# Kernel optimization log

Hardware: AMD Instinct MI355X
Metric: run time of the kernel (lower is better)

Reference implementation:

```python
import jax, jax.numpy as jnp
import numpy as np

SEQ = 2048
D_MODEL = 2048
N_HEADS = 16
D_HEAD = D_MODEL // N_HEADS
GN_EPS = 1e-5


def apply_xpos(x, inv=False, base=10000.0, scale_base=512.0):
    # x: (sqlen, d_head). Standard xPos: rotary embedding with exponential length scale.
    s, d = x.shape
    half = d // 2
    freqs = 1.0 / (base ** (jnp.arange(half, dtype=jnp.float32) / half))
    pos = jnp.arange(s, dtype=jnp.float32)
    ang = pos[:, None] * freqs[None, :]                       # (s, half)
    sin, cos = jnp.sin(ang), jnp.cos(ang)
    scale = ((jnp.arange(half, dtype=jnp.float32) + 0.4 * d) / (1.4 * d)) ** (pos[:, None] / scale_base)
    if inv:
        scale = 1.0 / scale
    x1, x2 = x[:, :half], x[:, half:]
    y1 = (x1 * cos - x2 * sin) * scale
    y2 = (x1 * sin + x2 * cos) * scale
    return jnp.concatenate([y1, y2], axis=-1)


def setup_inputs() -> dict:
    key = jax.random.key(0)
    ks = jax.random.split(key, 8)
    s = D_MODEL ** -0.5
    return {
        "x": jax.random.normal(ks[0], (SEQ, D_MODEL), jnp.float32),
        "state": jax.random.normal(ks[1], (N_HEADS, D_HEAD, D_HEAD), jnp.float32) * 0.1,
        "Wqkv": jax.random.normal(ks[2], (3 * D_MODEL, D_MODEL), jnp.float32) * s,
        "Walpha": jax.random.normal(ks[3], (1, D_MODEL), jnp.float32) * s,
        "gn_w": jnp.ones((D_MODEL,), jnp.float32),
        "gn_b": jnp.zeros((D_MODEL,), jnp.float32),
        "Wgate": jax.random.normal(ks[4], (D_MODEL, D_MODEL), jnp.float32) * s,
        "Wout": jax.random.normal(ks[5], (D_MODEL, D_MODEL), jnp.float32) * s,
    }


def reference(x, state, Wqkv, Walpha, gn_w, gn_b, Wgate, Wout):
    sqlen = x.shape[0]
    # qkv projection -> (3, H, s, Dh)
    qkv = (x @ Wqkv.T).reshape(sqlen, 3, N_HEADS, D_HEAD).transpose(1, 2, 0, 3)
    q, k, v = qkv[0], qkv[1], qkv[2]
    q = jax.vmap(apply_xpos)(q)
    k = jax.vmap(lambda t: apply_xpos(t, inv=True))(k)

    alphas = -jnp.log1p(jnp.exp(-(x @ Walpha.T)))             # log-sigmoid, (s, 1)
    k = (1.0 - jnp.exp(alphas)) * k                            # broadcast (s,1) over (H,s,Dh)
    a = jnp.cumsum(alphas, axis=0)                             # (s, 1)

    # Decay matrix; mask BEFORE exp (equivalent to tril-after since upper is zeroed,
    # but avoids overflow in exp for the upper triangle).
    tril = jnp.tril(jnp.ones((sqlen, sqlen), bool))
    Delta = jnp.exp(jnp.where(tril, a - a.T, -jnp.inf))        # (s, s)

    attn = jnp.tril(jnp.einsum('hid,hjd,ij->hij', q, k, Delta))  # (H, s, s)
    ret = jnp.einsum('hij,hjd->ihd', attn, v)                    # (s, H, Dh)

    new_state = jnp.exp(a[-1]) * state                           # (H, Dh, Dh)
    ret = ret + jnp.einsum('hid,hde->ihe', q, new_state)
    new_state = new_state + jnp.einsum('hid,hie,i->hde', k, v, jnp.exp(a[::-1, 0]))

    # GroupNorm(n_heads groups) over d_model, per token
    r = ret.reshape(sqlen, N_HEADS, D_HEAD)
    mu = r.mean(-1, keepdims=True)
    var = r.var(-1, keepdims=True)
    r = (r - mu) * jax.lax.rsqrt(var + GN_EPS)
    ret = r.reshape(sqlen, D_MODEL) * gn_w + gn_b

    gate = jax.nn.swish(ret @ Wgate.T)
    out = (gate * ret) @ Wout.T
    return out, new_state
```

## Files before the change

kernel.cpp:

```cpp
#include <hip/hip_runtime.h>

#define SEQ 2048
#define DM 2048
#define NH 16
#define DH 128

typedef float f32x4 __attribute__((ext_vector_type(4)));
typedef short s16x8 __attribute__((ext_vector_type(8)));

__device__ __forceinline__ ushort f2bf(float f) {
    unsigned u = __builtin_bit_cast(unsigned, f);
    return (ushort)((u + 0x7FFFu + ((u >> 16) & 1u)) >> 16);
}
__device__ __forceinline__ float bf2f(ushort u) {
    return __builtin_bit_cast(float, (unsigned)u << 16);
}
__device__ __forceinline__ void gload_lds16(const void* g, void* l) {
    __builtin_amdgcn_global_load_lds((const __attribute__((address_space(1))) void*)g,
                                     (__attribute__((address_space(3))) void*)l, 16, 0, 0);
}

__global__ __launch_bounds__(256) void k_xprep(const float* __restrict__ x,
                                               const float* __restrict__ wal,
                                               ushort* __restrict__ x_bf,
                                               float* __restrict__ z) {
    int row = blockIdx.x, t = threadIdx.x;
    const float4* xr = (const float4*)(x + (size_t)row * DM);
    const float4* wa = (const float4*)wal;
    float4 v0 = xr[t], v1 = xr[t + 256];
    float4 w0 = wa[t], w1 = wa[t + 256];
    float s = v0.x * w0.x + v0.y * w0.y + v0.z * w0.z + v0.w * w0.w
            + v1.x * w1.x + v1.y * w1.y + v1.z * w1.z + v1.w * w1.w;
    ushort4 o0, o1;
    o0.x = f2bf(v0.x); o0.y = f2bf(v0.y); o0.z = f2bf(v0.z); o0.w = f2bf(v0.w);
    o1.x = f2bf(v1.x); o1.y = f2bf(v1.y); o1.z = f2bf(v1.z); o1.w = f2bf(v1.w);
    ushort4* xb = (ushort4*)(x_bf + (size_t)row * DM);
    xb[t] = o0; xb[t + 256] = o1;
    __shared__ float red[4];
    int lane = t & 63, wv = t >> 6;
    #pragma unroll
    for (int off = 32; off; off >>= 1) s += __shfl_down(s, off);
    if (lane == 0) red[wv] = s;
    __syncthreads();
    if (t == 0) z[row] = red[0] + red[1] + red[2] + red[3];
}

__global__ __launch_bounds__(256) void k_prep2(const float* __restrict__ z,
                                               float* __restrict__ a,
                                               float* __restrict__ wrev,
                                               float* __restrict__ kscale,
                                               float* __restrict__ exp_alast,
                                               const float* __restrict__ Wqkv,
                                               ushort* __restrict__ Wqkv_bf,
                                               float* __restrict__ tsin,
                                               float* __restrict__ tcos,
                                               float* __restrict__ tsc) {
    int b = blockIdx.x, t = threadIdx.x;
    if (b == 0) {
        __shared__ float sh[SEQ];
        __shared__ float csum[256];
        for (int i = t; i < SEQ; i += 256) {
            float al = -log1pf(expf(-z[i]));
            sh[i] = al;
            kscale[i] = 1.f - expf(al);
        }
        __syncthreads();
        int base = t * 8;
        float run = 0.f, loc[8];
        #pragma unroll
        for (int j = 0; j < 8; j++) { run += sh[base + j]; loc[j] = run; }
        csum[t] = run;
        __syncthreads();
        if (t == 0) {
            float r = 0.f;
            for (int i = 0; i < 256; i++) { float v = csum[i]; csum[i] = r; r += v; }
        }
        __syncthreads();
        float off = csum[t];
        #pragma unroll
        for (int j = 0; j < 8; j++) { float av = loc[j] + off; sh[base + j] = av; a[base + j] = av; }
        __syncthreads();
        for (int i = t; i < SEQ; i += 256) wrev[i] = expf(sh[SEQ - 1 - i]);
        if (t == 0) *exp_alast = expf(sh[SEQ - 1]);
    } else if (b < 1 + 3 * DM * DM / 4 / 256) {
        int i = (b - 1) * 256 + t;
        float4 v = ((const float4*)Wqkv)[i];
        ushort4 o;
        o.x = f2bf(v.x); o.y = f2bf(v.y); o.z = f2bf(v.z); o.w = f2bf(v.w);
        ((ushort4*)Wqkv_bf)[i] = o;
    } else {
        int idx = (b - 1 - 3 * DM * DM / 4 / 256) * 256 + t;
        int i = idx >> 6, j = idx & 63;
        float freq = powf(10000.f, -(float)j / 64.f);
        float ang = (float)i * freq;
        tsin[idx] = sinf(ang);
        tcos[idx] = cosf(ang);
        tsc[idx]  = powf(((float)j + 51.2f) / 179.2f, (float)i / 512.f);
    }
}

template <int EPI, int STORE_BF16>
__global__ __launch_bounds__(256) void k_gemm_mfma(
    const ushort* __restrict__ A,
    const ushort* __restrict__ B,
    void* __restrict__ Cv, int ldc,
    const ushort* __restrict__ aux,
    int K)
{
    (void)K;
    __shared__ __align__(16) ushort As[128 * 64];
    __shared__ __align__(16) ushort Bs[128 * 64];
    int bx = blockIdx.x, by = blockIdx.y;
    {
        int id = by * 16 + bx;
        int xcd = id & 7, local = id >> 3;
        int lbx = local & 7, lby = local >> 3;
        bx = (xcd & 1) * 8 + lbx;
        by = (xcd >> 1) * 4 + lby;
    }
    int bm = by * 128, bn = bx * 128;
    int tid = threadIdx.x;
    int w = tid >> 6, l = tid & 63;
    int wr = w >> 1, wc = w & 1;
    int lr = l & 15, kg = l >> 4;

    int srow = w * 32 + (l >> 3);
    int scol = ((l & 7) ^ (l >> 3)) * 8;
    const ushort* ga = A + (size_t)(bm + srow) * DM + scol;
    const ushort* gb = B + (size_t)(bn + srow) * DM + scol;
    ushort* la = As + (w * 32) * 64;
    ushort* lb = Bs + (w * 32) * 64;

    f32x4 acc[4][4] = {};

    for (int k0 = 0; k0 < DM; k0 += 64) {
        __syncthreads();
        #pragma unroll
        for (int g = 0; g < 4; g++) {
            gload_lds16(ga + (size_t)(g * 8) * DM + k0, la + g * 8 * 64);
            gload_lds16(gb + (size_t)(g * 8) * DM + k0, lb + g * 8 * 64);
        }
        __syncthreads();

        #pragma unroll
        for (int kk = 0; kk < 2; kk++) {
            s16x8 af[4], bfr[4];
            #pragma unroll
            for (int m = 0; m < 4; m++) {
                int row = wr * 64 + m * 16 + lr;
                af[m] = *(const s16x8*)(As + row * 64 + (((kk * 4 + kg) ^ (lr & 7)) * 8));
            }
            #pragma unroll
            for (int n = 0; n < 4; n++) {
                int row = wc * 64 + n * 16 + lr;
                bfr[n] = *(const s16x8*)(Bs + row * 64 + (((kk * 4 + kg) ^ (lr & 7)) * 8));
            }
            #pragma unroll
            for (int m = 0; m < 4; m++)
                #pragma unroll
                for (int n = 0; n < 4; n++)
                    asm volatile("v_mfma_f32_16x16x32_bf16 %0, %1, %2, %0"
                                 : "+v"(acc[m][n]) : "v"(af[m]), "v"(bfr[n]));
        }
    }
    asm volatile("s_nop 7\n\ts_nop 7\n\ts_nop 7" ::: );

    #pragma unroll
    for (int m = 0; m < 4; m++) {
        int grow = bm + wr * 64 + m * 16 + kg * 4;
        #pragma unroll
        for (int n = 0; n < 4; n++) {
            int gcol = bn + wc * 64 + n * 16 + lr;
            #pragma unroll
            for (int j = 0; j < 4; j++) {
                float c = acc[m][n][j];
                size_t off = (size_t)(grow + j) * ldc + gcol;
                if (EPI == 1) {
                    float sig = 1.f / (1.f + __expf(-c));
                    c = c * sig * bf2f(aux[off]);
                }
                if (STORE_BF16) ((ushort*)Cv)[off] = f2bf(c);
                else            ((float*)Cv)[off] = c;
            }
        }
    }
}

__global__ __launch_bounds__(256) void k_gemm_qkv(
    const ushort* __restrict__ A,
    const ushort* __restrict__ B,
    const float* __restrict__ tsin,
    const float* __restrict__ tcos,
    const float* __restrict__ tsc,
    const float* __restrict__ kscale,
    const float* __restrict__ wrev,
    ushort* __restrict__ qh,
    ushort* __restrict__ kh,
    ushort* __restrict__ vth,
    ushort* __restrict__ kwtr)
{
    __shared__ __align__(16) char smem[33024];
    ushort* As = (ushort*)smem;
    ushort* Bs = (ushort*)(smem + 16384);
    int bx = blockIdx.x, by = blockIdx.y;
    {
        int id = by * 48 + bx;
        int xcd = id & 7, local = id >> 3;
        int lbx = local % 12, lby = local / 12;
        bx = (xcd & 3) * 12 + lbx;
        by = (xcd >> 2) * 8 + lby;
    }
    int bm = by * 128, bn = bx * 128;
    int tid = threadIdx.x;
    int w = tid >> 6, l = tid & 63;
    int wr = w >> 1, wc = w & 1;
    int lr = l & 15, kg = l >> 4;

    int srow = w * 32 + (l >> 3);
    int scol = ((l & 7) ^ (l >> 3)) * 8;
    const ushort* ga = A + (size_t)(bm + srow) * DM + scol;
    const ushort* gb = B + (size_t)(bn + srow) * DM + scol;
    ushort* la = As + (w * 32) * 64;
    ushort* lb = Bs + (w * 32) * 64;

    f32x4 acc[4][4] = {};

    for (int k0 = 0; k0 < DM; k0 += 64) {
        __syncthreads();
        #pragma unroll
        for (int g = 0; g < 4; g++) {
            gload_lds16(ga + (size_t)(g * 8) * DM + k0, la + g * 8 * 64);
            gload_lds16(gb + (size_t)(g * 8) * DM + k0, lb + g * 8 * 64);
        }
        __syncthreads();

        #pragma unroll
        for (int kk = 0; kk < 2; kk++) {
            s16x8 af[4], bfr[4];
            #pragma unroll
            for (int m = 0; m < 4; m++) {
                int row = wr * 64 + m * 16 + lr;
                af[m] = *(const s16x8*)(As + row * 64 + (((kk * 4 + kg) ^ (lr & 7)) * 8));
            }
            #pragma unroll
            for (int n = 0; n < 4; n++) {
                int row = wc * 64 + n * 16 + lr;
                bfr[n] = *(const s16x8*)(Bs + row * 64 + (((kk * 4 + kg) ^ (lr & 7)) * 8));
            }
            #pragma unroll
            for (int m = 0; m < 4; m++)
                #pragma unroll
                for (int n = 0; n < 4; n++)
                    asm volatile("v_mfma_f32_16x16x32_bf16 %0, %1, %2, %0"
                                 : "+v"(acc[m][n]) : "v"(af[m]), "v"(bfr[n]));
        }
    }
    asm volatile("s_nop 7\n\ts_nop 7\n\ts_nop 7" ::: );

    __syncthreads();
    ushort* S = (ushort*)smem;
    #pragma unroll
    for (int m = 0; m < 4; m++) {
        int row = wr * 64 + m * 16 + kg * 4;
        #pragma unroll
        for (int n = 0; n < 4; n++) {
            int col = wc * 64 + n * 16 + lr;
            #pragma unroll
            for (int j = 0; j < 4; j++)
                S[(row + j) * 129 + col] = f2bf(acc[m][n][j]);
        }
    }
    __syncthreads();

    int type = bn >> 11;
    int h = (bn & 2047) >> 7;

    if (type < 2) {
        #pragma unroll 4
        for (int rr = 0; rr < 32; rr++) {
            int r = w * 32 + rr;
            int i = bm + r;
            float sn = tsin[i * 64 + l], cs = tcos[i * 64 + l], sc = tsc[i * 64 + l];
            float v1 = bf2f(S[r * 129 + l]), v2 = bf2f(S[r * 129 + l + 64]);
            float r1 = v1 * cs - v2 * sn, r2 = v1 * sn + v2 * cs;
            size_t ob = ((size_t)h * SEQ + i) * DH;
            if (type == 0) {
                qh[ob + l]      = f2bf(r1 * sc);
                qh[ob + l + 64] = f2bf(r2 * sc);
            } else {
                float ks = kscale[i], wv = wrev[i];
                float isc = 1.f / sc;
                float k1 = r1 * isc * ks, k2 = r2 * isc * ks;
                kh[ob + l]      = f2bf(k1);
                kh[ob + l + 64] = f2bf(k2);
                S[r * 129 + l]      = f2bf(k1 * wv);
                S[r * 129 + l + 64] = f2bf(k2 * wv);
            }
        }
    }
    if (type >= 1) {
        __syncthreads();
        ushort* dstT = (type == 1) ? kwtr : vth;
        #pragma unroll 4
        for (int dd = 0; dd < 32; dd++) {
            int d = w * 32 + dd;
            ushort2 o;
            o.x = S[(2 * l) * 129 + d];
            o.y = S[(2 * l + 1) * 129 + d];
            *(ushort2*)(dstT + ((size_t)h * DH + d) * SEQ + bm + 2 * l) = o;
        }
    }
}

#define NUNITS 48
__constant__ unsigned char U_QT[NUNITS] = {
    31,31,30,15, 30,29,29,28,14, 28,27,27,26,13, 26,25,25,24,12,
    24,23,23,22,11, 22,21,21,20,10, 20,19,19,18,9, 18,17,17,16,8,
    16,7,6,5,4,3,2,1,0};
__constant__ unsigned char U_T0[NUNITS] = {
    0,16,0,0, 16,0,15,0,0, 15,0,14,0,0, 14,0,13,0,0,
    13,0,12,0,0, 12,0,11,0,0, 11,0,10,0,0, 10,0,9,0,0,
    9,0,0,0,0,0,0,0,0};
__constant__ unsigned char U_T1[NUNITS] = {
    16,32,16,16, 31,15,30,15,15, 29,14,28,14,14, 27,13,26,13,13,
    25,12,24,12,12, 23,11,22,11,11, 21,10,20,10,10, 19,9,18,9,9,
    17,8,7,6,5,4,3,2,1};

__global__ __launch_bounds__(256) void k_attn_mega(
    const ushort* __restrict__ qh,
    const ushort* __restrict__ kh,
    const ushort* __restrict__ vth,
    const ushort* __restrict__ kwtr,
    const float* __restrict__ a,
    float* __restrict__ ret,
    float* __restrict__ ret2,
    float* __restrict__ part,
    const float* __restrict__ gw,
    const float* __restrict__ gb,
    ushort* __restrict__ retn_bf,
    const float* __restrict__ Wgate,
    ushort* __restrict__ Wgate_bf,
    const float* __restrict__ Wout,
    ushort* __restrict__ Wout_bf)
{
    __shared__ __align__(16) char smem[81920];
    int h, u;
    {
        int id = blockIdx.y * NH + blockIdx.x;
        int xcd = id & 7, local = id >> 3;
        h = xcd * 2 + (local >> 6);
        u = local & 63;
    }
    int tid = threadIdx.x;
    int w = tid >> 6, l = tid & 63;
    int lr = l & 15, kg = l >> 4;

    if (u >= 56) {
        int id = (u - 56) * NH + h;
        const float4* g0 = (const float4*)Wgate;
        const float4* g1 = (const float4*)Wout;
        #pragma unroll 4
        for (int it = 0; it < 32; it++) {
            int idx = id * 8192 + it * 256 + tid;
            float4 v = g0[idx];
            ushort4 o;
            o.x = f2bf(v.x); o.y = f2bf(v.y); o.z = f2bf(v.z); o.w = f2bf(v.w);
            ((ushort4*)Wgate_bf)[idx] = o;
            v = g1[idx];
            o.x = f2bf(v.x); o.y = f2bf(v.y); o.z = f2bf(v.z); o.w = f2bf(v.w);
            ((ushort4*)Wout_bf)[idx] = o;
        }
        return;
    }
    if (u >= 48) {
        int ch = u - 48;
        const ushort* A = kwtr + (size_t)h * DH * SEQ + ch * (SEQ / 8);
        const ushort* B = vth  + (size_t)h * DH * SEQ + ch * (SEQ / 8);
        ushort* As = (ushort*)smem;
        ushort* Bs = (ushort*)(smem + 8192);
        int wr = w >> 1, wc = w & 1;
        int srow = w * 16 + (l >> 2);
        int scol = (l & 3) * 8;
        const ushort* ga0 = A + (size_t)srow * SEQ + scol;
        const ushort* ga1 = A + (size_t)(64 + srow) * SEQ + scol;
        const ushort* gb0 = B + (size_t)srow * SEQ + scol;
        const ushort* gb1 = B + (size_t)(64 + srow) * SEQ + scol;
        ushort* la0 = As + w * 512;
        ushort* la1 = As + 2048 + w * 512;
        ushort* lb0 = Bs + w * 512;
        ushort* lb1 = Bs + 2048 + w * 512;
        f32x4 acc[4][4] = {};
        for (int k0 = 0; k0 < SEQ / 8; k0 += 32) {
            __syncthreads();
            gload_lds16(ga0 + k0, la0);
            gload_lds16(ga1 + k0, la1);
            gload_lds16(gb0 + k0, lb0);
            gload_lds16(gb1 + k0, lb1);
            __syncthreads();
            s16x8 af[4], bfr[4];
            #pragma unroll
            for (int m = 0; m < 4; m++)
                af[m] = *(const s16x8*)(As + (wr * 64 + m * 16 + lr) * 32 + kg * 8);
            #pragma unroll
            for (int n = 0; n < 4; n++)
                bfr[n] = *(const s16x8*)(Bs + (wc * 64 + n * 16 + lr) * 32 + kg * 8);
            #pragma unroll
            for (int m = 0; m < 4; m++)
                #pragma unroll
                for (int n = 0; n < 4; n++)
                    asm volatile("v_mfma_f32_16x16x32_bf16 %0, %1, %2, %0"
                                 : "+v"(acc[m][n]) : "v"(af[m]), "v"(bfr[n]));
        }
        asm volatile("s_nop 7\n\ts_nop 7\n\ts_nop 7" ::: );
        float* p = part + ((size_t)ch * NH + h) * DH * DH;
        #pragma unroll
        for (int m = 0; m < 4; m++) {
            int grow = wr * 64 + m * 16 + kg * 4;
            #pragma unroll
            for (int n = 0; n < 4; n++) {
                int gcol = wc * 64 + n * 16 + lr;
                #pragma unroll
                for (int j = 0; j < 4; j++)
                    p[(size_t)(grow + j) * DH + gcol] = acc[m][n][j];
            }
        }
        return;
    }

    int qt = U_QT[u], t0 = U_T0[u], t1 = U_T1[u];
    int i0 = qt * 64;
    const ushort* Q  = qh  + (size_t)h * SEQ * DH;
    const ushort* K  = kh  + (size_t)h * SEQ * DH;
    const ushort* Vt = vth + (size_t)h * DH * SEQ;
#define KS(B) ((ushort*)(smem + (B) * 16384))
#define VS(B) ((ushort*)(smem + 32768 + (B) * 16384))
    char* Ps = smem + 65536;
    float* a_lds = (float*)(smem + 73728);

    int span = t1 * 64;
    for (int i = tid; i < span; i += 256) a_lds[i] = a[i];

    s16x8 qf[4];
    #pragma unroll
    for (int c = 0; c < 4; c++)
        qf[c] = *(const s16x8*)(Q + (size_t)(i0 + w * 16 + lr) * DH + c * 32 + kg * 8);
    float aq[4];
    #pragma unroll
    for (int r = 0; r < 4; r++) aq[r] = a[i0 + w * 16 + kg * 4 + r];

    f32x4 oacc[8] = {};

#define STAGE(T, B) do { int j0_ = (T) * 64;                                      \
    _Pragma("unroll") for (int g = 0; g < 4; g++) {                               \
        int row = w * 16 + g * 4 + (l >> 4);                                      \
        int cb = ((l & 15) * 16) ^ ((row & 7) << 4);                              \
        gload_lds16(K + (size_t)(j0_ + row) * DH + cb / 2,                        \
                    (char*)KS(B) + (w * 16 + g * 4) * 256); }                     \
    _Pragma("unroll") for (int g = 0; g < 4; g++) {                               \
        int e = w * 32 + g * 8 + (l >> 3);                                        \
        int cb = ((l & 7) * 16) ^ ((e & 7) << 4);                                 \
        gload_lds16(Vt + (size_t)e * SEQ + j0_ + cb / 2,                          \
                    (char*)VS(B) + (w * 32 + g * 8) * 128); }                     \
} while (0)

    STAGE(t0, 0);
    __syncthreads();

    for (int t = t0; t < t1; t++) {
        int cur = (t - t0) & 1;
        if (t + 1 < t1) {
            STAGE(t + 1, cur ^ 1);
            asm volatile("s_waitcnt vmcnt(8)" ::: "memory");
        } else {
            asm volatile("s_waitcnt vmcnt(0)" ::: "memory");
        }
        __builtin_amdgcn_s_barrier();

        f32x4 sacc[4] = {};
        __builtin_amdgcn_s_setprio(1);
        #pragma unroll
        for (int n = 0; n < 4; n++) {
            int krow = n * 16 + lr;
            #pragma unroll
            for (int c = 0; c < 4; c++) {
                s16x8 kf = *(const s16x8*)((const char*)KS(cur) + krow * 256 +
                            ((c * 64 + kg * 16) ^ ((krow & 7) << 4)));
                asm volatile("v_mfma_f32_16x16x32_bf16 %0, %1, %2, %0"
                             : "+v"(sacc[n]) : "v"(qf[c]), "v"(kf));
            }
        }
        __builtin_amdgcn_s_setprio(0);
        asm volatile("s_nop 7\n\ts_nop 7" ::: );

        int j0 = t * 64;
        float aref = a_lds[j0];
        float ei[4], ej[4];
        #pragma unroll
        for (int r = 0; r < 4; r++) ei[r] = __expf(aq[r] - aref);
        #pragma unroll
        for (int n = 0; n < 4; n++) ej[n] = __expf(aref - a_lds[j0 + n * 16 + lr]);
        bool diag = (t == qt);
        #pragma unroll
        for (int n = 0; n < 4; n++) {
            #pragma unroll
            for (int r = 0; r < 4; r++) {
                float wv = ei[r] * ej[n];
                if (diag)
                    wv = (n * 16 + lr <= w * 16 + kg * 4 + r) ? wv : 0.f;
                float p = sacc[n][r] * wv;
                int prow = w * 16 + kg * 4 + r;
                *(ushort*)(Ps + prow * 128 +
                           (((n * 16 + lr) * 2) ^ ((prow & 7) << 4))) = f2bf(p);
            }
        }
        __builtin_amdgcn_s_setprio(1);
        #pragma unroll
        for (int c2 = 0; c2 < 2; c2++) {
            int prow = w * 16 + lr;
            s16x8 pf = *(const s16x8*)((const char*)Ps + prow * 128 +
                        ((c2 * 64 + kg * 16) ^ ((prow & 7) << 4)));
            #pragma unroll
            for (int n2 = 0; n2 < 8; n2++) {
                int erow = n2 * 16 + lr;
                s16x8 vf = *(const s16x8*)((const char*)VS(cur) + erow * 128 +
                            ((c2 * 64 + kg * 16) ^ ((erow & 7) << 4)));
                asm volatile("v_mfma_f32_16x16x32_bf16 %0, %1, %2, %0"
                             : "+v"(oacc[n2]) : "v"(pf), "v"(vf));
            }
        }
        __builtin_amdgcn_s_setprio(0);
        asm volatile("s_waitcnt lgkmcnt(0)" ::: "memory");
        __builtin_amdgcn_s_barrier();
    }
#undef STAGE
    asm volatile("s_nop 7\n\ts_nop 7\n\ts_nop 7" ::: );

    if (qt < 16) {
        float gwr[8], gbr[8];
        #pragma unroll
        for (int n2 = 0; n2 < 8; n2++) {
            gwr[n2] = gw[h * DH + n2 * 16 + lr];
            gbr[n2] = gb[h * DH + n2 * 16 + lr];
        }
        #pragma unroll
        for (int j = 0; j < 4; j++) {
            float s = 0.f, sq = 0.f;
            #pragma unroll
            for (int n2 = 0; n2 < 8; n2++) { float v = oacc[n2][j]; s += v; sq += v * v; }
            #pragma unroll
            for (int off = 8; off; off >>= 1) {
                s  += __shfl_xor(s, off);
                sq += __shfl_xor(sq, off);
            }
            float mu = s * (1.f / 128.f);
            float var = sq * (1.f / 128.f) - mu * mu;
            float inv = rsqrtf(var + 1e-5f);
            int gi = i0 + w * 16 + kg * 4 + j;
            #pragma unroll
            for (int n2 = 0; n2 < 8; n2++) {
                float val = (oacc[n2][j] - mu) * inv * gwr[n2] + gbr[n2];
                retn_bf[(size_t)gi * DM + h * DH + n2 * 16 + lr] = f2bf(val);
            }
        }
    } else {
        float* dst = (t0 == 0) ? ret + (size_t)i0 * DM
                               : ret2 + (size_t)(i0 - 1024) * DM;
        #pragma unroll
        for (int n2 = 0; n2 < 8; n2++) {
            #pragma unroll
            for (int j = 0; j < 4; j++) {
                int ri = w * 16 + kg * 4 + j;
                dst[(size_t)ri * DM + h * DH + n2 * 16 + lr] = oacc[n2][j];
            }
        }
    }
}

__global__ __launch_bounds__(64) void k_gnorm(const float* __restrict__ ret,
                                              const float* __restrict__ ret2,
                                              const float* __restrict__ gw,
                                              const float* __restrict__ gb,
                                              ushort* __restrict__ retn_bf,
                                              const float* __restrict__ part,
                                              const float* __restrict__ state,
                                              const float* __restrict__ exp_alast,
                                              float* __restrict__ out_state) {
    int bx = blockIdx.x, h = blockIdx.y;
    int t = threadIdx.x;
    if (bx >= 1024) {
        int bx2 = bx - 1024;
        int idx4 = bx2 * 64 + t;
        size_t off = (size_t)h * (DH * DH / 4) + idx4;
        float ea = *exp_alast;
        float4 s4 = ((const float4*)state)[off];
        float4 acc;
        acc.x = s4.x * ea; acc.y = s4.y * ea; acc.z = s4.z * ea; acc.w = s4.w * ea;
        #pragma unroll
        for (int ch = 0; ch < 8; ch++) {
            float4 p4 = ((const float4*)part)[((size_t)ch * NH) * (DH * DH / 4) + off];
            acc.x += p4.x; acc.y += p4.y; acc.z += p4.z; acc.w += p4.w;
        }
        ((float4*)out_state)[off] = acc;
        return;
    }
    int i = 1024 + bx;
    const float* r = ret + (size_t)i * DM + h * DH;
    const float* r2 = ret2 + (size_t)(i - 1024) * DM + h * DH;
    float v0 = r[t] + r2[t], v1 = r[t + 64] + r2[t + 64];
    float s = v0 + v1, sq = v0 * v0 + v1 * v1;
    #pragma unroll
    for (int off = 32; off; off >>= 1) { s += __shfl_xor(s, off); sq += __shfl_xor(sq, off); }
    float mu = s * (1.f / 128.f);
    float var = sq * (1.f / 128.f) - mu * mu;
    float inv = rsqrtf(var + 1e-5f);
    ushort* o = retn_bf + (size_t)i * DM + h * DH;
    o[t]      = f2bf((v0 - mu) * inv * gw[h * DH + t]      + gb[h * DH + t]);
    o[t + 64] = f2bf((v1 - mu) * inv * gw[h * DH + t + 64] + gb[h * DH + t + 64]);
}

extern "C" void kernel_launch(void* const* d_in, const int* in_sizes, int n_in,
                              void* d_out, int out_size, void* d_ws, size_t ws_size,
                              hipStream_t stream) {
    (void)in_sizes; (void)n_in; (void)out_size; (void)ws_size;
    const float* x      = (const float*)d_in[0];
    const float* state  = (const float*)d_in[1];
    const float* Wqkv   = (const float*)d_in[2];
    const float* Walpha = (const float*)d_in[3];
    const float* gn_w   = (const float*)d_in[4];
    const float* gn_b   = (const float*)d_in[5];
    const float* Wgate  = (const float*)d_in[6];
    const float* Wout   = (const float*)d_in[7];
    float* out       = (float*)d_out;
    float* out_state = out + (size_t)SEQ * DM;

    char* base = (char*)d_ws;
    ushort* x_bf     = (ushort*)base;
    ushort* retn_bf  = (ushort*)base;
    ushort* Wqkv_bf  = (ushort*)(base + 8388608);
    float*  ret      = (float*)(base + 8388608);
    float*  ret2     = (float*)(base + 25165824);
    ushort* qh       = (ushort*)(base + 33554432);
    ushort* kh       = (ushort*)(base + 41943040);
    ushort* vth      = (ushort*)(base + 50331648);
    ushort* kwtr     = (ushort*)(base + 58720256);
    float*  part     = (float*)(base + 67108864);
    ushort* gr_bf    = (ushort*)(base + 67108864);
    float*  tsin     = (float*)(base + 75497472);
    float*  tcos     = (float*)(base + 75497472 + 524288);
    float*  tsc      = (float*)(base + 75497472 + 1048576);
    ushort* Wgate_bf = (ushort*)(base + 75497472);
    ushort* Wout_bf  = (ushort*)(base + 83886080);
    float*  smalls   = (float*)(base + 92274688);
    float* z = smalls, *a = z + SEQ, *wrev = a + SEQ, *kscale = wrev + SEQ, *exp_alast = kscale + SEQ;

    k_xprep<<<dim3(SEQ), dim3(256), 0, stream>>>(x, Walpha, x_bf, z);
    k_prep2<<<dim3(1 + 3 * DM * DM / 4 / 256 + SEQ * 64 / 256), dim3(256), 0, stream>>>(
        z, a, wrev, kscale, exp_alast, Wqkv, Wqkv_bf, tsin, tcos, tsc);
    k_gemm_qkv<<<dim3(48, SEQ / 128), dim3(256), 0, stream>>>(
        x_bf, Wqkv_bf, tsin, tcos, tsc, kscale, wrev, qh, kh, vth, kwtr);
    k_attn_mega<<<dim3(NH, 64), dim3(256), 0, stream>>>(
        qh, kh, vth, kwtr, a, ret, ret2, part,
        gn_w, gn_b, retn_bf, Wgate, Wgate_bf, Wout, Wout_bf);
    k_gnorm<<<dim3(1024 + 64, NH), dim3(64), 0, stream>>>(
        ret, ret2, gn_w, gn_b, retn_bf, part, state, exp_alast, out_state);
    k_gemm_mfma<1, 1><<<dim3(DM / 128, SEQ / 128), dim3(256), 0, stream>>>(
        retn_bf, Wgate_bf, gr_bf, DM, retn_bf, DM);
    k_gemm_mfma<0, 0><<<dim3(DM / 128, SEQ / 128), dim3(256), 0, stream>>>(
        gr_bf, Wout_bf, out, DM, nullptr, DM);
}
```

Before: 222.4 us.

## Fuse prep kernels and group-norm into producers via last-block atomic counters

New measurement: 447.2 us. 101% more time.

```diff
diff --git a/kernel.cpp b/kernel.cpp
--- a/kernel.cpp
+++ b/kernel.cpp
@@ -20,76 +20,84 @@
                                      (__attribute__((address_space(3))) void*)l, 16, 0, 0);
 }
 
-__global__ __launch_bounds__(256) void k_xprep(const float* __restrict__ x,
-                                               const float* __restrict__ wal,
-                                               ushort* __restrict__ x_bf,
-                                               float* __restrict__ z) {
-    int row = blockIdx.x, t = threadIdx.x;
-    const float4* xr = (const float4*)(x + (size_t)row * DM);
-    const float4* wa = (const float4*)wal;
-    float4 v0 = xr[t], v1 = xr[t + 256];
-    float4 w0 = wa[t], w1 = wa[t + 256];
-    float s = v0.x * w0.x + v0.y * w0.y + v0.z * w0.z + v0.w * w0.w
-            + v1.x * w1.x + v1.y * w1.y + v1.z * w1.z + v1.w * w1.w;
-    ushort4 o0, o1;
-    o0.x = f2bf(v0.x); o0.y = f2bf(v0.y); o0.z = f2bf(v0.z); o0.w = f2bf(v0.w);
-    o1.x = f2bf(v1.x); o1.y = f2bf(v1.y); o1.z = f2bf(v1.z); o1.w = f2bf(v1.w);
-    ushort4* xb = (ushort4*)(x_bf + (size_t)row * DM);
-    xb[t] = o0; xb[t + 256] = o1;
+__global__ __launch_bounds__(256) void k_mega_prep(
+    const float* __restrict__ x,
+    const float* __restrict__ wal,
+    ushort* __restrict__ x_bf,
+    float* __restrict__ z,
+    const float* __restrict__ Wqkv,
+    ushort* __restrict__ Wqkv_bf,
+    float* __restrict__ tsin,
+    float* __restrict__ tcos,
+    float* __restrict__ tsc,
+    float* __restrict__ a,
+    float* __restrict__ wrev,
+    float* __restrict__ kscale,
+    float* __restrict__ exp_alast,
+    int* __restrict__ ctrs)
+{
+    __shared__ float sh[SEQ];
+    __shared__ float csum[256];
     __shared__ float red[4];
-    int lane = t & 63, wv = t >> 6;
-    #pragma unroll
-    for (int off = 32; off; off >>= 1) s += __shfl_down(s, off);
-    if (lane == 0) red[wv] = s;
-    __syncthreads();
-    if (t == 0) z[row] = red[0] + red[1] + red[2] + red[3];
-}
-
-__global__ __launch_bounds__(256) void k_prep2(const float* __restrict__ z,
-                                               float* __restrict__ a,
-                                               float* __restrict__ wrev,
-                                               float* __restrict__ kscale,
-                                               float* __restrict__ exp_alast,
-                                               const float* __restrict__ Wqkv,
-                                               ushort* __restrict__ Wqkv_bf,
-                                               float* __restrict__ tsin,
-                                               float* __restrict__ tcos,
-                                               float* __restrict__ tsc) {
+    __shared__ int amLast;
     int b = blockIdx.x, t = threadIdx.x;
-    if (b == 0) {
-        __shared__ float sh[SEQ];
-        __shared__ float csum[256];
-        for (int i = t; i < SEQ; i += 256) {
-            float al = -log1pf(expf(-z[i]));
-            sh[i] = al;
-            kscale[i] = 1.f - expf(al);
-        }
-        __syncthreads();
-        int base = t * 8;
-        float run = 0.f, loc[8];
-        #pragma unroll
-        for (int j = 0; j < 8; j++) { run += sh[base + j]; loc[j] = run; }
-        csum[t] = run;
+    if (b < SEQ) {
+        const float4* xr = (const float4*)(x + (size_t)b * DM);
+        const float4* wa = (const float4*)wal;
+        float4 v0 = xr[t], v1 = xr[t + 256];
+        float4 w0 = wa[t], w1 = wa[t + 256];
+        float s = v0.x * w0.x + v0.y * w0.y + v0.z * w0.z + v0.w * w0.w
+                + v1.x * w1.x + v1.y * w1.y + v1.z * w1.z + v1.w * w1.w;
+        ushort4 o0, o1;
+        o0.x = f2bf(v0.x); o0.y = f2bf(v0.y); o0.z = f2bf(v0.z); o0.w = f2bf(v0.w);
+        o1.x = f2bf(v1.x); o1.y = f2bf(v1.y); o1.z = f2bf(v1.z); o1.w = f2bf(v1.w);
+        ushort4* xb = (ushort4*)(x_bf + (size_t)b * DM);
+        xb[t] = o0; xb[t + 256] = o1;
+        int lane = t & 63, wv = t >> 6;
+        #pragma unroll
+        for (int off = 32; off; off >>= 1) s += __shfl_down(s, off);
+        if (lane == 0) red[wv] = s;
         __syncthreads();
         if (t == 0) {
-            float r = 0.f;
-            for (int i = 0; i < 256; i++) { float v = csum[i]; csum[i] = r; r += v; }
-        }
-        __syncthreads();
-        float off = csum[t];
-        #pragma unroll
-        for (int j = 0; j < 8; j++) { float av = loc[j] + off; sh[base + j] = av; a[base + j] = av; }
-        __syncthreads();
-        for (int i = t; i < SEQ; i += 256) wrev[i] = expf(sh[SEQ - 1 - i]);
-        if (t == 0) *exp_alast = expf(sh[SEQ - 1]);
-    } else if (b < 1 + 3 * DM * DM / 4 / 256) {
-        int i = (b - 1) * 256 + t;
+            z[b] = red[0] + red[1] + red[2] + red[3];
+            __threadfence();
+            amLast = (atomicAdd(&ctrs[0], 1) == SEQ - 1);
+        }
+        __syncthreads();
+        if (amLast) {
+            __threadfence();
+            for (int i = t; i < SEQ; i += 256) {
+                float al = -log1pf(expf(-z[i]));
+                sh[i] = al;
+                kscale[i] = 1.f - expf(al);
+            }
+            __syncthreads();
+            int base = t * 8;
+            float run = 0.f, loc[8];
+            #pragma unroll
+            for (int j = 0; j < 8; j++) { run += sh[base + j]; loc[j] = run; }
+            csum[t] = run;
+            __syncthreads();
+            if (t == 0) {
+                float r = 0.f;
+                for (int i = 0; i < 256; i++) { float v = csum[i]; csum[i] = r; r += v; }
+            }
+            __syncthreads();
+            float off = csum[t];
+            #pragma unroll
+            for (int j = 0; j < 8; j++) { float av = loc[j] + off; sh[base + j] = av; a[base + j] = av; }
+            __syncthreads();
+            for (int i = t; i < SEQ; i += 256) wrev[i] = expf(sh[SEQ - 1 - i]);
+            if (t == 0) *exp_alast = expf(sh[SEQ - 1]);
+        }
+    } else if (b < SEQ + 3 * DM * DM / 4 / 256) {
+        int i = (b - SEQ) * 256 + t;
         float4 v = ((const float4*)Wqkv)[i];
         ushort4 o;
         o.x = f2bf(v.x); o.y = f2bf(v.y); o.z = f2bf(v.z); o.w = f2bf(v.w);
         ((ushort4*)Wqkv_bf)[i] = o;
     } else {
-        int idx = (b - 1 - 3 * DM * DM / 4 / 256) * 256 + t;
+        int idx = (b - SEQ - 3 * DM * DM / 4 / 256) * 256 + t;
         int i = idx >> 6, j = idx & 63;
         float freq = powf(10000.f, -(float)j / 64.f);
         float ang = (float)i * freq;
@@ -341,9 +349,14 @@
     const float* __restrict__ Wgate,
     ushort* __restrict__ Wgate_bf,
     const float* __restrict__ Wout,
-    ushort* __restrict__ Wout_bf)
+    ushort* __restrict__ Wout_bf,
+    const float* __restrict__ state,
+    const float* __restrict__ exp_alast,
+    float* __restrict__ out_state,
+    int* __restrict__ ctrs)
 {
     __shared__ __align__(16) char smem[81920];
+    __shared__ int amLast;
     int h, u;
     {
         int id = blockIdx.y * NH + blockIdx.x;
@@ -424,6 +437,28 @@
                     p[(size_t)(grow + j) * DH + gcol] = acc[m][n][j];
             }
         }
+        __threadfence();
+        if (tid == 0) amLast = (atomicAdd(&ctrs[272 + h], 1) == 7);
+        __syncthreads();
+        if (amLast) {
+            __threadfence();
+            float ea = *exp_alast;
+            #pragma unroll 4
+            for (int it = 0; it < 16; it++) {
+                int idx4 = it * 256 + tid;
+                size_t off2 = (size_t)h * 4096 + idx4;
+                float4 s4 = ((const float4*)state)[off2];
+                float4 acc2;
+                acc2.x = s4.x * ea; acc2.y = s4.y * ea;
+                acc2.z = s4.z * ea; acc2.w = s4.w * ea;
+                #pragma unroll
+                for (int c2 = 0; c2 < 8; c2++) {
+                    float4 p4 = ((const float4*)part)[(size_t)c2 * NH * 4096 + off2];
+                    acc2.x += p4.x; acc2.y += p4.y; acc2.z += p4.z; acc2.w += p4.w;
+                }
+                ((float4*)out_state)[off2] = acc2;
+            }
+        }
         return;
     }
 
@@ -573,49 +608,34 @@
                 dst[(size_t)ri * DM + h * DH + n2 * 16 + lr] = oacc[n2][j];
             }
         }
-    }
-}
-
-__global__ __launch_bounds__(64) void k_gnorm(const float* __restrict__ ret,
-                                              const float* __restrict__ ret2,
-                                              const float* __restrict__ gw,
-                                              const float* __restrict__ gb,
-                                              ushort* __restrict__ retn_bf,
-                                              const float* __restrict__ part,
-                                              const float* __restrict__ state,
-                                              const float* __restrict__ exp_alast,
-                                              float* __restrict__ out_state) {
-    int bx = blockIdx.x, h = blockIdx.y;
-    int t = threadIdx.x;
-    if (bx >= 1024) {
-        int bx2 = bx - 1024;
-        int idx4 = bx2 * 64 + t;
-        size_t off = (size_t)h * (DH * DH / 4) + idx4;
-        float ea = *exp_alast;
-        float4 s4 = ((const float4*)state)[off];
-        float4 acc;
-        acc.x = s4.x * ea; acc.y = s4.y * ea; acc.z = s4.z * ea; acc.w = s4.w * ea;
-        #pragma unroll
-        for (int ch = 0; ch < 8; ch++) {
-            float4 p4 = ((const float4*)part)[((size_t)ch * NH) * (DH * DH / 4) + off];
-            acc.x += p4.x; acc.y += p4.y; acc.z += p4.z; acc.w += p4.w;
-        }
-        ((float4*)out_state)[off] = acc;
-        return;
-    }
-    int i = 1024 + bx;
-    const float* r = ret + (size_t)i * DM + h * DH;
-    const float* r2 = ret2 + (size_t)(i - 1024) * DM + h * DH;
-    float v0 = r[t] + r2[t], v1 = r[t + 64] + r2[t + 64];
-    float s = v0 + v1, sq = v0 * v0 + v1 * v1;
-    #pragma unroll
-    for (int off = 32; off; off >>= 1) { s += __shfl_xor(s, off); sq += __shfl_xor(sq, off); }
-    float mu = s * (1.f / 128.f);
-    float var = sq * (1.f / 128.f) - mu * mu;
-    float inv = rsqrtf(var + 1e-5f);
-    ushort* o = retn_bf + (size_t)i * DM + h * DH;
-    o[t]      = f2bf((v0 - mu) * inv * gw[h * DH + t]      + gb[h * DH + t]);
-    o[t + 64] = f2bf((v1 - mu) * inv * gw[h * DH + t + 64] + gb[h * DH + t + 64]);
+        __threadfence();
+        if (tid == 0) amLast = (atomicAdd(&ctrs[16 + h * 16 + (qt - 16)], 1) == 1);
+        __syncthreads();
+        if (amLast) {
+            __threadfence();
+            float gw0 = gw[h * DH + l], gw1 = gw[h * DH + l + 64];
+            float gb0 = gb[h * DH + l], gb1 = gb[h * DH + l + 64];
+            for (int rr = 0; rr < 16; rr++) {
+                int i = i0 + w * 16 + rr;
+                const float* r  = ret  + (size_t)i * DM + h * DH;
+                const float* r2 = ret2 + (size_t)(i - 1024) * DM + h * DH;
+                float v0 = r[l] + r2[l];
+                float v1 = r[l + 64] + r2[l + 64];
+                float s = v0 + v1, sq = v0 * v0 + v1 * v1;
+                #pragma unroll
+                for (int off = 32; off; off >>= 1) {
+                    s  += __shfl_xor(s, off);
+                    sq += __shfl_xor(sq, off);
+                }
+                float mu = s * (1.f / 128.f);
+                float var = sq * (1.f / 128.f) - mu * mu;
+                float inv = rsqrtf(var + 1e-5f);
+                ushort* o = retn_bf + (size_t)i * DM + h * DH;
+                o[l]      = f2bf((v0 - mu) * inv * gw0 + gb0);
+                o[l + 64] = f2bf((v1 - mu) * inv * gw1 + gb1);
+            }
+        }
+    }
 }
 
 extern "C" void kernel_launch(void* const* d_in, const int* in_sizes, int n_in,
@@ -652,17 +672,18 @@
     ushort* Wout_bf  = (ushort*)(base + 83886080);
     float*  smalls   = (float*)(base + 92274688);
     float* z = smalls, *a = z + SEQ, *wrev = a + SEQ, *kscale = wrev + SEQ, *exp_alast = kscale + SEQ;
-
-    k_xprep<<<dim3(SEQ), dim3(256), 0, stream>>>(x, Walpha, x_bf, z);
-    k_prep2<<<dim3(1 + 3 * DM * DM / 4 / 256 + SEQ * 64 / 256), dim3(256), 0, stream>>>(
-        z, a, wrev, kscale, exp_alast, Wqkv, Wqkv_bf, tsin, tcos, tsc);
+    int*   ctrs      = (int*)(base + 92274688 + 36864);
+
+    hipMemsetAsync(ctrs, 0, 4096, stream);
+    k_mega_prep<<<dim3(SEQ + 3 * DM * DM / 4 / 256 + SEQ * 64 / 256), dim3(256), 0, stream>>>(
+        x, Walpha, x_bf, z, Wqkv, Wqkv_bf, tsin, tcos, tsc,
+        a, wrev, kscale, exp_alast, ctrs);
     k_gemm_qkv<<<dim3(48, SEQ / 128), dim3(256), 0, stream>>>(
         x_bf, Wqkv_bf, tsin, tcos, tsc, kscale, wrev, qh, kh, vth, kwtr);
     k_attn_mega<<<dim3(NH, 64), dim3(256), 0, stream>>>(
         qh, kh, vth, kwtr, a, ret, ret2, part,
-        gn_w, gn_b, retn_bf, Wgate, Wgate_bf, Wout, Wout_bf);
-    k_gnorm<<<dim3(1024 + 64, NH), dim3(64), 0, stream>>>(
-        ret, ret2, gn_w, gn_b, retn_bf, part, state, exp_alast, out_state);
+        gn_w, gn_b, retn_bf, Wgate, Wgate_bf, Wout, Wout_bf,
+        state, exp_alast, out_state, ctrs);
     k_gemm_mfma<1, 1><<<dim3(DM / 128, SEQ / 128), dim3(256), 0, stream>>>(
         retn_bf, Wgate_bf, gr_bf, DM, retn_bf, DM);
     k_gemm_mfma<0, 0><<<dim3(DM / 128, SEQ / 128), dim3(256), 0, stream>>>(
```

## Move Wout bf16 conversion into QKV GEMM launch and widen gnorm blocks

Applied to the files above, without the earlier changes.

Result: no change. 223.1 us (+0.4%).

```diff
diff --git a/kernel.cpp b/kernel.cpp
--- a/kernel.cpp
+++ b/kernel.cpp
@@ -197,21 +197,36 @@
     ushort* __restrict__ qh,
     ushort* __restrict__ kh,
     ushort* __restrict__ vth,
-    ushort* __restrict__ kwtr)
+    ushort* __restrict__ kwtr,
+    const float* __restrict__ Wout,
+    ushort* __restrict__ Wout_bf)
 {
+    int tid = threadIdx.x;
+    if (blockIdx.x >= 768) {
+        int cid = blockIdx.x - 768;
+        const float4* g1 = (const float4*)Wout;
+        #pragma unroll 4
+        for (int it = 0; it < 64; it++) {
+            int idx = cid * 16384 + it * 256 + tid;
+            float4 v = g1[idx];
+            ushort4 o;
+            o.x = f2bf(v.x); o.y = f2bf(v.y); o.z = f2bf(v.z); o.w = f2bf(v.w);
+            ((ushort4*)Wout_bf)[idx] = o;
+        }
+        return;
+    }
     __shared__ __align__(16) char smem[33024];
     ushort* As = (ushort*)smem;
     ushort* Bs = (ushort*)(smem + 16384);
-    int bx = blockIdx.x, by = blockIdx.y;
+    int bx, by;
     {
-        int id = by * 48 + bx;
+        int id = blockIdx.x;
         int xcd = id & 7, local = id >> 3;
         int lbx = local % 12, lby = local / 12;
         bx = (xcd & 3) * 12 + lbx;
         by = (xcd >> 2) * 8 + lby;
     }
     int bm = by * 128, bn = bx * 128;
-    int tid = threadIdx.x;
     int w = tid >> 6, l = tid & 63;
     int wr = w >> 1, wc = w & 1;
     int lr = l & 15, kg = l >> 4;
@@ -339,36 +354,30 @@
     const float* __restrict__ gb,
     ushort* __restrict__ retn_bf,
     const float* __restrict__ Wgate,
-    ushort* __restrict__ Wgate_bf,
-    const float* __restrict__ Wout,
-    ushort* __restrict__ Wout_bf)
+    ushort* __restrict__ Wgate_bf)
 {
     __shared__ __align__(16) char smem[81920];
     int h, u;
     {
         int id = blockIdx.y * NH + blockIdx.x;
         int xcd = id & 7, local = id >> 3;
-        h = xcd * 2 + (local >> 6);
-        u = local & 63;
+        h = xcd * 2 + (local / 60);
+        u = local % 60;
     }
     int tid = threadIdx.x;
     int w = tid >> 6, l = tid & 63;
     int lr = l & 15, kg = l >> 4;
 
     if (u >= 56) {
-        int id = (u - 56) * NH + h;
+        int s = (u - 56) * NH + h;
         const float4* g0 = (const float4*)Wgate;
-        const float4* g1 = (const float4*)Wout;
         #pragma unroll 4
-        for (int it = 0; it < 32; it++) {
-            int idx = id * 8192 + it * 256 + tid;
+        for (int it = 0; it < 64; it++) {
+            int idx = s * 16384 + it * 256 + tid;
             float4 v = g0[idx];
             ushort4 o;
             o.x = f2bf(v.x); o.y = f2bf(v.y); o.z = f2bf(v.z); o.w = f2bf(v.w);
             ((ushort4*)Wgate_bf)[idx] = o;
-            v = g1[idx];
-            o.x = f2bf(v.x); o.y = f2bf(v.y); o.z = f2bf(v.z); o.w = f2bf(v.w);
-            ((ushort4*)Wout_bf)[idx] = o;
         }
         return;
     }
@@ -576,37 +585,41 @@
     }
 }
 
-__global__ __launch_bounds__(64) void k_gnorm(const float* __restrict__ ret,
-                                              const float* __restrict__ ret2,
-                                              const float* __restrict__ gw,
-                                              const float* __restrict__ gb,
-                                              ushort* __restrict__ retn_bf,
-                                              const float* __restrict__ part,
-                                              const float* __restrict__ state,
-                                              const float* __restrict__ exp_alast,
-                                              float* __restrict__ out_state) {
+__global__ __launch_bounds__(256) void k_gnorm(const float* __restrict__ ret,
+                                               const float* __restrict__ ret2,
+                                               const float* __restrict__ gw,
+                                               const float* __restrict__ gb,
+                                               ushort* __restrict__ retn_bf,
+                                               const float* __restrict__ part,
+                                               const float* __restrict__ state,
+                                               const float* __restrict__ exp_alast,
+                                               float* __restrict__ out_state) {
     int bx = blockIdx.x, h = blockIdx.y;
     int t = threadIdx.x;
-    if (bx >= 1024) {
-        int bx2 = bx - 1024;
-        int idx4 = bx2 * 64 + t;
-        size_t off = (size_t)h * (DH * DH / 4) + idx4;
+    if (bx >= 256) {
+        int bx2 = bx - 256;
         float ea = *exp_alast;
-        float4 s4 = ((const float4*)state)[off];
-        float4 acc;
-        acc.x = s4.x * ea; acc.y = s4.y * ea; acc.z = s4.z * ea; acc.w = s4.w * ea;
-        #pragma unroll
-        for (int ch = 0; ch < 8; ch++) {
-            float4 p4 = ((const float4*)part)[((size_t)ch * NH) * (DH * DH / 4) + off];
-            acc.x += p4.x; acc.y += p4.y; acc.z += p4.z; acc.w += p4.w;
-        }
-        ((float4*)out_state)[off] = acc;
+        #pragma unroll
+        for (int it = 0; it < 4; it++) {
+            int idx4 = bx2 * 1024 + it * 256 + t;
+            size_t off = (size_t)h * (DH * DH / 4) + idx4;
+            float4 s4 = ((const float4*)state)[off];
+            float4 acc;
+            acc.x = s4.x * ea; acc.y = s4.y * ea; acc.z = s4.z * ea; acc.w = s4.w * ea;
+            #pragma unroll
+            for (int ch = 0; ch < 8; ch++) {
+                float4 p4 = ((const float4*)part)[((size_t)ch * NH) * (DH * DH / 4) + off];
+                acc.x += p4.x; acc.y += p4.y; acc.z += p4.z; acc.w += p4.w;
+            }
+            ((float4*)out_state)[off] = acc;
+        }
         return;
     }
-    int i = 1024 + bx;
+    int wv = t >> 6, l = t & 63;
+    int i = 1024 + bx * 4 + wv;
     const float* r = ret + (size_t)i * DM + h * DH;
     const float* r2 = ret2 + (size_t)(i - 1024) * DM + h * DH;
-    float v0 = r[t] + r2[t], v1 = r[t + 64] + r2[t + 64];
+    float v0 = r[l] + r2[l], v1 = r[l + 64] + r2[l + 64];
     float s = v0 + v1, sq = v0 * v0 + v1 * v1;
     #pragma unroll
     for (int off = 32; off; off >>= 1) { s += __shfl_xor(s, off); sq += __shfl_xor(sq, off); }
@@ -614,8 +627,8 @@
     float var = sq * (1.f / 128.f) - mu * mu;
     float inv = rsqrtf(var + 1e-5f);
     ushort* o = retn_bf + (size_t)i * DM + h * DH;
-    o[t]      = f2bf((v0 - mu) * inv * gw[h * DH + t]      + gb[h * DH + t]);
-    o[t + 64] = f2bf((v1 - mu) * inv * gw[h * DH + t + 64] + gb[h * DH + t + 64]);
+    o[l]      = f2bf((v0 - mu) * inv * gw[h * DH + l]      + gb[h * DH + l]);
+    o[l + 64] = f2bf((v1 - mu) * inv * gw[h * DH + l + 64] + gb[h * DH + l + 64]);
 }
 
 extern "C" void kernel_launch(void* const* d_in, const int* in_sizes, int n_in,
@@ -656,12 +669,13 @@
     k_xprep<<<dim3(SEQ), dim3(256), 0, stream>>>(x, Walpha, x_bf, z);
     k_prep2<<<dim3(1 + 3 * DM * DM / 4 / 256 + SEQ * 64 / 256), dim3(256), 0, stream>>>(
         z, a, wrev, kscale, exp_alast, Wqkv, Wqkv_bf, tsin, tcos, tsc);
-    k_gemm_qkv<<<dim3(48, SEQ / 128), dim3(256), 0, stream>>>(
-        x_bf, Wqkv_bf, tsin, tcos, tsc, kscale, wrev, qh, kh, vth, kwtr);
-    k_attn_mega<<<dim3(NH, 64), dim3(256), 0, stream>>>(
+    k_gemm_qkv<<<dim3(832), dim3(256), 0, stream>>>(
+        x_bf, Wqkv_bf, tsin, tcos, tsc, kscale, wrev, qh, kh, vth, kwtr,
+        Wout, Wout_bf);
+    k_attn_mega<<<dim3(NH, 60), dim3(256), 0, stream>>>(
         qh, kh, vth, kwtr, a, ret, ret2, part,
-        gn_w, gn_b, retn_bf, Wgate, Wgate_bf, Wout, Wout_bf);
-    k_gnorm<<<dim3(1024 + 64, NH), dim3(64), 0, stream>>>(
+        gn_w, gn_b, retn_bf, Wgate, Wgate_bf);
+    k_gnorm<<<dim3(256 + 4, NH), dim3(256), 0, stream>>>(
         ret, ret2, gn_w, gn_b, retn_bf, part, state, exp_alast, out_state);
     k_gemm_mfma<1, 1><<<dim3(DM / 128, SEQ / 128), dim3(256), 0, stream>>>(
         retn_bf, Wgate_bf, gr_bf, DM, retn_bf, DM);
```
